# Kernel optimization log

Hardware: AMD Instinct MI355X
Metric: run time of the kernel (lower is better)

## Reference

```python
import jax, jax.numpy as jnp
import numpy as np

B, T, V, R = 512, 24, 32000, 32
# Scale keeps both the selected chain (factor ~ sqrt(R)*c per step) and the
# vocab-marginalized chain (factor ~ sqrt(V*R)*c per step) inside fp32 range.
CORE_SCALE = (R * np.sqrt(V)) ** -0.5


def setup_inputs() -> dict:
    key = jax.random.key(0)
    k1, k2, k3, k4 = jax.random.split(key, 4)
    y = jax.random.randint(k1, (B, T), 0, V)                      # (B, T) token ids
    alpha = jax.random.normal(k2, (1, R), dtype=jnp.float32)      # left boundary
    beta = jax.random.normal(k3, (1, R), dtype=jnp.float32)       # right boundary
    core = jax.random.normal(k4, (1, R, V, R), dtype=jnp.float32) * CORE_SCALE
    return {"y": y, "alpha": alpha, "beta": beta, "core": core}


def _mps_fwd(alpha, beta, core, y):
    a = alpha[0]                                   # (R,)
    b = beta[0]                                    # (R,)
    cores = jnp.transpose(core[0], (1, 0, 2))      # (V, R, R): per-token transfer matrices
    bsz, seq = y.shape

    # --- unnormalized p(y): chain of selected R x R matrices (marginalize_mask = 0) ---
    sel = jnp.moveaxis(cores[y], 1, 0)             # (T, B, R, R) gathered transfer matrices
    init = jnp.broadcast_to(a, (bsz, R))           # (B, R)

    def step(state, M):                            # state: (B, R), M: (B, R, R)
        return jnp.einsum('br,brs->bs', state, M), None

    state, _ = jax.lax.scan(step, init, sel)
    p_tilde = state @ b                            # (B,)

    # --- normalization: every position marginalized over vocab (free pos-0 leg also summed) ---
    m = cores.sum(axis=0)                          # (R, R) marginalized transfer matrix

    def zstep(v, _):                               # v: (R,)
        return v @ m, None

    vz, _ = jax.lax.scan(zstep, a, None, length=seq)
    z = (vz @ b) * bsz                             # z_one is identical per row; .sum() over batch

    return jnp.concatenate([p_tilde, z[None]])     # (B + 1,): [p_tilde..., z]


def reference(y, alpha, beta, core):
    return _mps_fwd(alpha, beta, core, y)
```

## Files before the change

kernel.cpp:

```cpp
#include <hip/hip_runtime.h>

#define RNK 32
#define VOC 32000
#define BSZ 512
#define SEQ 24
#define HSEQ 12

#define LEFT_BLOCKS  BSZ
#define CHAIN_BLOCKS (2 * BSZ)
#define RED_CHUNKS 125
#define REDUCE_BLOCKS (32 * RED_CHUNKS)
#define DEPTH 4
#define NSLOT 5

typedef const __attribute__((address_space(1))) void* as1_cvp;
typedef __attribute__((address_space(3))) void* as3_vp;

__device__ __forceinline__ void issue_matrix_load(const float* src_tok,
                                                  float* lds_base, int lane) {
    const int rlo = lane >> 3;
    const int cq  = ((lane & 7) ^ rlo) * 4;
    #pragma unroll
    for (int j = 0; j < 4; ++j) {
        const float* src = src_tok + (size_t)(j * 8 + rlo) * ((size_t)VOC * RNK) + cq;
        __builtin_amdgcn_global_load_lds((as1_cvp)src, (as3_vp)(lds_base + j * 256), 16, 0, 0);
    }
}

__global__ __launch_bounds__(64) void fused_kernel(const float* __restrict__ core,
                                                   const int* __restrict__ y,
                                                   const float* __restrict__ alpha,
                                                   const float* __restrict__ beta,
                                                   float* __restrict__ Lv,
                                                   float* __restrict__ Rv,
                                                   float* __restrict__ gm) {
    __shared__ float mbuf[NSLOT * 1024];
    const int tid = threadIdx.x;

    if (blockIdx.x < CHAIN_BLOCKS) {
        const bool right = blockIdx.x >= LEFT_BLOCKS;
        const int  row   = blockIdx.x - (right ? LEFT_BLOCKS : 0);
        const int  lane  = tid;
        const int  s     = lane & 31;
        const int  half  = lane >> 5;

        int ytok = 0;
        if (lane < HSEQ) ytok = y[row * SEQ + (right ? (SEQ - 1 - lane) : lane)];

        float state = right ? beta[s] : alpha[s];

        int la[16];
        if (!right) {
            #pragma unroll
            for (int i = 0; i < 16; ++i) {
                const int r = half * 16 + i;
                la[i] = r * 32 + ((((s >> 2) ^ (r & 7)) ) << 2) + (s & 3);
            }
        } else {
            #pragma unroll
            for (int i = 0; i < 16; ++i) {
                la[i] = s * 32 + ((((half * 4 + (i >> 2)) ^ (s & 7))) << 2) + (i & 3);
            }
        }

        asm volatile("s_waitcnt vmcnt(0)" ::: "memory");

        #pragma unroll
        for (int pt = 0; pt < DEPTH; ++pt) {
            const int tok = __shfl(ytok, pt, 64);
            issue_matrix_load(core + (size_t)tok * RNK, mbuf + pt * 1024, lane);
        }

        #pragma unroll
        for (int t = 0; t < HSEQ; ++t) {
            if      (t <= HSEQ - 4) asm volatile("s_waitcnt vmcnt(12)" ::: "memory");
            else if (t == HSEQ - 3) asm volatile("s_waitcnt vmcnt(8)"  ::: "memory");
            else if (t == HSEQ - 2) asm volatile("s_waitcnt vmcnt(4)"  ::: "memory");
            else                    asm volatile("s_waitcnt vmcnt(0)"  ::: "memory");
            __builtin_amdgcn_sched_barrier(0);

            const float* M = mbuf + (t % NSLOT) * 1024;
            float a0 = 0.f, a1 = 0.f, a2 = 0.f, a3 = 0.f;
            #pragma unroll
            for (int i = 0; i < 16; i += 4) {
                a0 = fmaf(__shfl(state, half * 16 + i + 0, 64), M[la[i + 0]], a0);
                a1 = fmaf(__shfl(state, half * 16 + i + 1, 64), M[la[i + 1]], a1);
                a2 = fmaf(__shfl(state, half * 16 + i + 2, 64), M[la[i + 2]], a2);
                a3 = fmaf(__shfl(state, half * 16 + i + 3, 64), M[la[i + 3]], a3);
            }
            const float acc = (a0 + a1) + (a2 + a3);
            state = acc + __shfl_xor(acc, 32, 64);

            if (t + DEPTH < HSEQ) {
                const int tok = __shfl(ytok, t + DEPTH, 64);
                issue_matrix_load(core + (size_t)tok * RNK,
                                  mbuf + ((t + DEPTH) % NSLOT) * 1024, lane);
            }
        }

        if (lane < 32) (right ? Rv : Lv)[row * RNK + lane] = state;
    } else {
        const int bid   = blockIdx.x - CHAIN_BLOCKS;
        const int r     = bid & 31;
        const int chunk = bid >> 5;

        const float4* slab = (const float4*)(core + (size_t)r * VOC * RNK);
        const int base = chunk * 2048 + tid;

        float a0 = 0.f, a1 = 0.f, a2 = 0.f, a3 = 0.f;
        #pragma unroll
        for (int i = 0; i < 32; ++i) {
            float4 v = slab[base + i * 64];
            a0 += v.x; a1 += v.y; a2 += v.z; a3 += v.w;
        }

        #pragma unroll
        for (int mask = 8; mask <= 32; mask <<= 1) {
            a0 += __shfl_xor(a0, mask, 64);
            a1 += __shfl_xor(a1, mask, 64);
            a2 += __shfl_xor(a2, mask, 64);
            a3 += __shfl_xor(a3, mask, 64);
        }
        if (tid < 8) {
            const int s0 = tid * 4;
            atomicAdd(&gm[r * RNK + s0 + 0], a0);
            atomicAdd(&gm[r * RNK + s0 + 1], a1);
            atomicAdd(&gm[r * RNK + s0 + 2], a2);
            atomicAdd(&gm[r * RNK + s0 + 3], a3);
        }
    }
}

__global__ __launch_bounds__(256) void dotz_kernel(const float* __restrict__ Lv,
                                                   const float* __restrict__ Rv,
                                                   const float* __restrict__ gm,
                                                   const float* __restrict__ alpha,
                                                   const float* __restrict__ beta,
                                                   float* __restrict__ out) {
    if (blockIdx.x < 64) {
        const int row = blockIdx.x * 8 + (threadIdx.x >> 5);
        const int l   = threadIdx.x & 31;
        float v = Lv[row * RNK + l] * Rv[row * RNK + l];
        #pragma unroll
        for (int m = 16; m >= 1; m >>= 1) v += __shfl_xor(v, m, 64);
        if (l == 0) out[row] = v;
    } else if (threadIdx.x < 64) {
        const int s    = threadIdx.x & 31;
        const int half = threadIdx.x >> 5;
        float col[16];
        #pragma unroll
        for (int i = 0; i < 16; ++i) col[i] = gm[(half * 16 + i) * RNK + s];
        float v = alpha[s];
        #pragma unroll
        for (int t = 0; t < SEQ; ++t) {
            float a0 = 0.f, a1 = 0.f, a2 = 0.f, a3 = 0.f;
            #pragma unroll
            for (int i = 0; i < 16; i += 4) {
                a0 = fmaf(__shfl(v, half * 16 + i + 0, 64), col[i + 0], a0);
                a1 = fmaf(__shfl(v, half * 16 + i + 1, 64), col[i + 1], a1);
                a2 = fmaf(__shfl(v, half * 16 + i + 2, 64), col[i + 2], a2);
                a3 = fmaf(__shfl(v, half * 16 + i + 3, 64), col[i + 3], a3);
            }
            const float acc = (a0 + a1) + (a2 + a3);
            v = acc + __shfl_xor(acc, 32, 64);
        }
        float z = v * beta[s];
        #pragma unroll
        for (int m = 16; m >= 1; m >>= 1) z += __shfl_xor(z, m, 64);
        if (threadIdx.x == 0) out[BSZ] = z * (float)BSZ;
    }
}

extern "C" void kernel_launch(void* const* d_in, const int* in_sizes, int n_in,
                              void* d_out, int out_size, void* d_ws, size_t ws_size,
                              hipStream_t stream) {
    const int*   y     = (const int*)d_in[0];
    const float* alpha = (const float*)d_in[1];
    const float* beta  = (const float*)d_in[2];
    const float* core  = (const float*)d_in[3];
    float* out = (float*)d_out;
    float* gm  = (float*)d_ws;
    float* Lv  = gm + RNK * RNK;
    float* Rv  = Lv + BSZ * RNK;

    hipMemsetAsync(gm, 0, RNK * RNK * sizeof(float), stream);
    fused_kernel<<<CHAIN_BLOCKS + REDUCE_BLOCKS, 64, 0, stream>>>(
        core, y, alpha, beta, Lv, Rv, gm);
    dotz_kernel<<<65, 256, 0, stream>>>(Lv, Rv, gm, alpha, beta, out);
}
```

Measured before the change: 45.27 us.

## Prefetch all chain matrices upfront across two waves instead of software pipelining

Chain blocks grow to 128 threads. Each wave issues half of the twelve per-token matrix loads into a 12-slot LDS buffer, then both waves wait, sync and run the chain redundantly from LDS. This replaces the 4-deep rolling prefetch with its staged vmcnt waits. Reduction blocks are widened to 128 threads, each thread handling half as many float4 loads. The cost is a 48KB static LDS allocation that also applies to the reduction blocks, which cuts blocks per CU. The chain no longer overlaps its loads with compute.

```diff
diff --git a/kernel.cpp b/kernel.cpp
--- a/kernel.cpp
+++ b/kernel.cpp
@@ -10,8 +10,7 @@
 #define CHAIN_BLOCKS (2 * BSZ)
 #define RED_CHUNKS 125
 #define REDUCE_BLOCKS (32 * RED_CHUNKS)
-#define DEPTH 4
-#define NSLOT 5
+#define BLOCK 128
 
 typedef const __attribute__((address_space(1))) void* as1_cvp;
 typedef __attribute__((address_space(3))) void* as3_vp;
@@ -27,20 +26,21 @@
     }
 }
 
-__global__ __launch_bounds__(64) void fused_kernel(const float* __restrict__ core,
-                                                   const int* __restrict__ y,
-                                                   const float* __restrict__ alpha,
-                                                   const float* __restrict__ beta,
-                                                   float* __restrict__ Lv,
-                                                   float* __restrict__ Rv,
-                                                   float* __restrict__ gm) {
-    __shared__ float mbuf[NSLOT * 1024];
-    const int tid = threadIdx.x;
+__global__ __launch_bounds__(BLOCK) void fused_kernel(const float* __restrict__ core,
+                                                      const int* __restrict__ y,
+                                                      const float* __restrict__ alpha,
+                                                      const float* __restrict__ beta,
+                                                      float* __restrict__ Lv,
+                                                      float* __restrict__ Rv,
+                                                      float* __restrict__ gm) {
+    __shared__ float mbuf[HSEQ * 1024];
+    const int tid  = threadIdx.x;
+    const int lane = tid & 63;
+    const int w    = tid >> 6;
 
     if (blockIdx.x < CHAIN_BLOCKS) {
         const bool right = blockIdx.x >= LEFT_BLOCKS;
         const int  row   = blockIdx.x - (right ? LEFT_BLOCKS : 0);
-        const int  lane  = tid;
         const int  s     = lane & 31;
         const int  half  = lane >> 5;
 
@@ -54,32 +54,27 @@
             #pragma unroll
             for (int i = 0; i < 16; ++i) {
                 const int r = half * 16 + i;
-                la[i] = r * 32 + ((((s >> 2) ^ (r & 7)) ) << 2) + (s & 3);
+                la[i] = r * 32 + (((s >> 2) ^ (r & 7)) << 2) + (s & 3);
             }
         } else {
             #pragma unroll
             for (int i = 0; i < 16; ++i) {
-                la[i] = s * 32 + ((((half * 4 + (i >> 2)) ^ (s & 7))) << 2) + (i & 3);
+                la[i] = s * 32 + (((half * 4 + (i >> 2)) ^ (s & 7)) << 2) + (i & 3);
             }
         }
 
+        #pragma unroll
+        for (int pt = 0; pt < 6; ++pt) {
+            const int slot = 6 * w + pt;
+            const int tok  = __shfl(ytok, slot, 64);
+            issue_matrix_load(core + (size_t)tok * RNK, mbuf + slot * 1024, lane);
+        }
         asm volatile("s_waitcnt vmcnt(0)" ::: "memory");
-
-        #pragma unroll
-        for (int pt = 0; pt < DEPTH; ++pt) {
-            const int tok = __shfl(ytok, pt, 64);
-            issue_matrix_load(core + (size_t)tok * RNK, mbuf + pt * 1024, lane);
-        }
+        __syncthreads();
 
         #pragma unroll
         for (int t = 0; t < HSEQ; ++t) {
-            if      (t <= HSEQ - 4) asm volatile("s_waitcnt vmcnt(12)" ::: "memory");
-            else if (t == HSEQ - 3) asm volatile("s_waitcnt vmcnt(8)"  ::: "memory");
-            else if (t == HSEQ - 2) asm volatile("s_waitcnt vmcnt(4)"  ::: "memory");
-            else                    asm volatile("s_waitcnt vmcnt(0)"  ::: "memory");
-            __builtin_amdgcn_sched_barrier(0);
-
-            const float* M = mbuf + (t % NSLOT) * 1024;
+            const float* M = mbuf + t * 1024;
             float a0 = 0.f, a1 = 0.f, a2 = 0.f, a3 = 0.f;
             #pragma unroll
             for (int i = 0; i < 16; i += 4) {
@@ -90,15 +85,9 @@
             }
             const float acc = (a0 + a1) + (a2 + a3);
             state = acc + __shfl_xor(acc, 32, 64);
-
-            if (t + DEPTH < HSEQ) {
-                const int tok = __shfl(ytok, t + DEPTH, 64);
-                issue_matrix_load(core + (size_t)tok * RNK,
-                                  mbuf + ((t + DEPTH) % NSLOT) * 1024, lane);
-            }
         }
 
-        if (lane < 32) (right ? Rv : Lv)[row * RNK + lane] = state;
+        if (tid < 32) (right ? Rv : Lv)[row * RNK + tid] = state;
     } else {
         const int bid   = blockIdx.x - CHAIN_BLOCKS;
         const int r     = bid & 31;
@@ -109,8 +98,8 @@
 
         float a0 = 0.f, a1 = 0.f, a2 = 0.f, a3 = 0.f;
         #pragma unroll
-        for (int i = 0; i < 32; ++i) {
-            float4 v = slab[base + i * 64];
+        for (int i = 0; i < 16; ++i) {
+            float4 v = slab[base + i * 128];
             a0 += v.x; a1 += v.y; a2 += v.z; a3 += v.w;
         }
 
@@ -121,8 +110,8 @@
             a2 += __shfl_xor(a2, mask, 64);
             a3 += __shfl_xor(a3, mask, 64);
         }
-        if (tid < 8) {
-            const int s0 = tid * 4;
+        if ((tid & 63) < 8) {
+            const int s0 = (tid & 7) * 4;
             atomicAdd(&gm[r * RNK + s0 + 0], a0);
             atomicAdd(&gm[r * RNK + s0 + 1], a1);
             atomicAdd(&gm[r * RNK + s0 + 2], a2);
@@ -184,7 +173,7 @@
     float* Rv  = Lv + BSZ * RNK;
 
     hipMemsetAsync(gm, 0, RNK * RNK * sizeof(float), stream);
-    fused_kernel<<<CHAIN_BLOCKS + REDUCE_BLOCKS, 64, 0, stream>>>(
+    fused_kernel<<<CHAIN_BLOCKS + REDUCE_BLOCKS, BLOCK, 0, stream>>>(
         core, y, alpha, beta, Lv, Rv, gm);
     dotz_kernel<<<65, 256, 0, stream>>>(Lv, Rv, gm, alpha, beta, out);
 }
```

After: 56.25 us. +24.3%, slower.
